# Optimization experiments

Hardware: AMD Instinct MI355X
Metric: run time of the kernel (lower is better)

## Reference

```python
import jax, jax.numpy as jnp
import numpy as np
import math

EMB, HEAD, B, S = 1024, 64, 4, 4096

def setup_inputs() -> dict:
    key = jax.random.key(0)
    ks = jax.random.split(key, 7)
    scale = 1.0 / math.sqrt(EMB)
    return {
        "x": jax.random.normal(ks[0], (B, S, EMB), dtype=jnp.float32),
        "Wq": jax.random.uniform(ks[1], (EMB, HEAD), jnp.float32, -scale, scale),
        "bq": jax.random.uniform(ks[2], (HEAD,), jnp.float32, -scale, scale),
        "Wk": jax.random.uniform(ks[3], (EMB, HEAD), jnp.float32, -scale, scale),
        "bk": jax.random.uniform(ks[4], (HEAD,), jnp.float32, -scale, scale),
        "Wv": jax.random.uniform(ks[5], (EMB, HEAD), jnp.float32, -scale, scale),
        "bv": jax.random.uniform(ks[6], (HEAD,), jnp.float32, -scale, scale),
    }

def reference(x, Wq, bq, Wk, bk, Wv, bv):
    # x: [B, S, E]
    q = x @ Wq + bq            # [B, S, H]
    k = x @ Wk + bk
    v = x @ Wv + bv
    scores = jnp.einsum('bqh,bkh->bqk', q, k) / math.sqrt(q.shape[-1])
    # causal mask: position q attends to k <= q
    s = x.shape[1]
    causal = jnp.tril(jnp.ones((s, s), dtype=bool))
    scores = jnp.where(causal, scores, -jnp.inf)
    attn = jax.nn.softmax(scores, axis=-1)
    return jnp.einsum('bqk,bkh->bqh', attn, v)
```

## Files before the change

kernel.cpp:

```cpp
#include <hip/hip_runtime.h>
#include <hip/hip_bf16.h>
#include <math.h>

#define EMB 1024
#define HEAD 64
#define NB 4
#define SEQ 4096
#define MTOT (NB * SEQ)
#define QSCALE (0.125f * 1.44269504088896f)

typedef __attribute__((ext_vector_type(8))) short bf16x8;
typedef __attribute__((ext_vector_type(4))) float f32x4;
typedef __attribute__((ext_vector_type(16))) float f32x16;

static __device__ __forceinline__ unsigned short f2b(float f) {
    union { float f; unsigned u; } v; v.f = f;
    unsigned r = v.u + 0x7FFFu + ((v.u >> 16) & 1u);
    return (unsigned short)(r >> 16);
}
static __device__ __forceinline__ float b2f(unsigned short u) {
    union { unsigned u; float f; } v; v.u = ((unsigned)u) << 16; return v.f;
}
static __device__ __forceinline__ unsigned pk2(float lo, float hi) {
    unsigned r;
    asm("v_cvt_pk_bf16_f32 %0, %1, %2" : "=v"(r) : "v"(lo), "v"(hi));
    return r;
}

__global__ void wt_kernel(const float* __restrict__ Wq, const float* __restrict__ Wk,
                          const float* __restrict__ Wv, unsigned short* __restrict__ Wt) {
    const int idx = blockIdx.x * 256 + threadIdx.x;
    const int m = idx >> 16;
    const int r = idx & 65535;
    const int n = r >> 10, k = r & 1023;
    const float* W = (m == 0) ? Wq : (m == 1) ? Wk : Wv;
    Wt[idx] = f2b(W[k * HEAD + n]);
}

__global__ __launch_bounds__(256) void proj_kernel(
    const float* __restrict__ x, const unsigned short* __restrict__ Wt3,
    const float* __restrict__ bq, const float* __restrict__ bk,
    const float* __restrict__ bv, unsigned short* __restrict__ qg,
    unsigned short* __restrict__ kb, unsigned short* __restrict__ vb) {
    __shared__ unsigned short Ax[32][72];
    __shared__ unsigned short Wl[192][72];

    const int tid = threadIdx.x;
    const int wave = tid >> 6, lane = tid & 63;
    const int li = lane & 15, lg = lane >> 4;
    const int rbase = blockIdx.x * 32;

    f32x4 acc[2][3];
#pragma unroll
    for (int m = 0; m < 2; ++m)
#pragma unroll
        for (int n = 0; n < 3; ++n) acc[m][n] = (f32x4){0.f, 0.f, 0.f, 0.f};

    const int xr = tid >> 3, xc = (tid & 7) * 8;

    for (int k0 = 0; k0 < EMB; k0 += 64) {
        __syncthreads();
        const float* xp = x + (size_t)(rbase + xr) * EMB + k0 + xc;
        const float4 t0 = *(const float4*)(xp);
        const float4 t1 = *(const float4*)(xp + 4);
        union { bf16x8 v; unsigned u[4]; } pa;
        pa.u[0] = pk2(t0.x, t0.y); pa.u[1] = pk2(t0.z, t0.w);
        pa.u[2] = pk2(t1.x, t1.y); pa.u[3] = pk2(t1.z, t1.w);
        *(bf16x8*)&Ax[xr][xc] = pa.v;
#pragma unroll
        for (int i = 0; i < 6; ++i) {
            const int chunk = tid + 256 * i;
            const int row = chunk >> 3, c8 = (chunk & 7) * 8;
            *(bf16x8*)&Wl[row][c8] = *(const bf16x8*)(Wt3 + (size_t)row * EMB + k0 + c8);
        }
        __syncthreads();

        const bf16x8 a0 = *(const bf16x8*)&Ax[li][lg * 8];
        const bf16x8 a1 = *(const bf16x8*)&Ax[li][32 + lg * 8];
        const bf16x8 a2 = *(const bf16x8*)&Ax[16 + li][lg * 8];
        const bf16x8 a3 = *(const bf16x8*)&Ax[16 + li][32 + lg * 8];
#pragma unroll
        for (int n = 0; n < 3; ++n) {
            const bf16x8 b0 = *(const bf16x8*)&Wl[(wave * 3 + n) * 16 + li][lg * 8];
            const bf16x8 b1 = *(const bf16x8*)&Wl[(wave * 3 + n) * 16 + li][32 + lg * 8];
            acc[0][n] = __builtin_amdgcn_mfma_f32_16x16x32_bf16(a0, b0, acc[0][n], 0, 0, 0);
            acc[0][n] = __builtin_amdgcn_mfma_f32_16x16x32_bf16(a1, b1, acc[0][n], 0, 0, 0);
            acc[1][n] = __builtin_amdgcn_mfma_f32_16x16x32_bf16(a2, b0, acc[1][n], 0, 0, 0);
            acc[1][n] = __builtin_amdgcn_mfma_f32_16x16x32_bf16(a3, b1, acc[1][n], 0, 0, 0);
        }
    }
#pragma unroll
    for (int m = 0; m < 2; ++m)
#pragma unroll
        for (int n = 0; n < 3; ++n) {
            const int f = wave * 3 + n;
            const int mat = f >> 2;
            const int nc = (f & 3) * 16 + li;
            const float bb = (mat == 0) ? bq[nc] : (mat == 1) ? bk[nc] : bv[nc];
#pragma unroll
            for (int r = 0; r < 4; ++r) {
                const int grow = rbase + m * 16 + lg * 4 + r;
                const float val = acc[m][n][r] + bb;
                const int bi = grow >> 12, si = grow & 4095;
                if (mat == 0) {
                    qg[(size_t)grow * HEAD + nc] = f2b(val * QSCALE);
                } else if (mat == 1) {
                    kb[((size_t)(bi * 2 + ((nc >> 3) & 1)) * 4 + (nc >> 4)) * (SEQ * 8)
                       + (size_t)si * 8 + (nc & 7)] = f2b(val);
                } else {
                    vb[((size_t)(bi * 512 + (si >> 3))) * 512 + (size_t)nc * 8 + (si & 7)] = f2b(val);
                }
            }
        }
}

template<int W64, int NWIN, int KMAX>
__global__ __launch_bounds__(256) void attn_kernel(
    const unsigned short* __restrict__ Qg, const unsigned short* __restrict__ Kb,
    const unsigned short* __restrict__ Vb, unsigned* __restrict__ pO,
    float* __restrict__ pML) {
    const int lane = threadIdx.x & 63;
    const int ql = lane & 31, h = lane >> 5;
    const int b = blockIdx.y;
    const int w = blockIdx.x * 4 + (threadIdx.x >> 6);
    int seg = 0;
#pragma unroll
    for (int kk = 1; kk < KMAX; ++kk)
        if (w >= 128 * kk - W64 * kk * (kk - 1)) seg = kk;
    const int Os = 128 * seg - W64 * seg * (seg - 1);
    const int qidx = 2 * W64 * seg + (w - Os);
    const int tdiag = qidx >> 1;
    const int qa0 = qidx * 32;
    const int t0 = W64 * seg;
    const int tend = (t0 + W64 < tdiag + 1) ? t0 + W64 : tdiag + 1;

    const size_t qb = (size_t)b * SEQ * HEAD;
    const unsigned short* kb0 = Kb + ((size_t)(b * 2 + h)) * 4 * (SEQ * 8);
    const unsigned short* vb0 = Vb + (size_t)b * 512 * 512;

    const unsigned short* qrow = Qg + qb + (size_t)(qa0 + ql) * HEAD + h * 8;
    bf16x8 qf[4];
#pragma unroll
    for (int s = 0; s < 4; ++s) qf[s] = *(const bf16x8*)(qrow + s * 16);

    f32x16 oa0, oa1;
#pragma unroll
    for (int r = 0; r < 16; ++r) { oa0[r] = 0.f; oa1[r] = 0.f; }
    float m = -1e30f, lsum = 0.f;

    bf16x8 kcur[2][4], knxt[2][4];
#pragma unroll
    for (int hh = 0; hh < 2; ++hh)
#pragma unroll
        for (int s = 0; s < 4; ++s)
            kcur[hh][s] = *(const bf16x8*)(kb0 + (size_t)s * (SEQ * 8)
                                           + ((size_t)t0 * 64 + 32 * hh + ql) * 8);

    for (int t = t0; t < tend; ++t) {
        bf16x8 vf[2][4];
#pragma unroll
        for (int dt = 0; dt < 2; ++dt)
#pragma unroll
            for (int cc = 0; cc < 4; ++cc)
                vf[dt][cc] = *(const bf16x8*)(vb0 + ((size_t)t * 8 + 2 * cc + h) * 512
                                              + (dt * 32 + ql) * 8);

        f32x16 st0, st1;
#pragma unroll
        for (int r = 0; r < 16; ++r) { st0[r] = 0.f; st1[r] = 0.f; }
        __builtin_amdgcn_s_setprio(1);
#pragma unroll
        for (int s = 0; s < 4; ++s) {
            st0 = __builtin_amdgcn_mfma_f32_32x32x16_bf16(kcur[0][s], qf[s], st0, 0, 0, 0);
            st1 = __builtin_amdgcn_mfma_f32_32x32x16_bf16(kcur[1][s], qf[s], st1, 0, 0, 0);
        }
        __builtin_amdgcn_s_setprio(0);

        if (t + 1 < tend) {
#pragma unroll
            for (int hh = 0; hh < 2; ++hh)
#pragma unroll
                for (int s = 0; s < 4; ++s)
                    knxt[hh][s] = *(const bf16x8*)(kb0 + (size_t)s * (SEQ * 8)
                                                   + ((size_t)(t + 1) * 64 + 32 * hh + ql) * 8);
        }

        if (t == tdiag) {
            if (qidx & 1) {
#pragma unroll
                for (int r = 0; r < 16; ++r) {
                    const int kvl = (r & 3) + 8 * (r >> 2) + 4 * h;
                    if (kvl > ql) st1[r] = -1e30f;
                }
            } else {
#pragma unroll
                for (int r = 0; r < 16; ++r) {
                    const int kvl = (r & 3) + 8 * (r >> 2) + 4 * h;
                    if (kvl > ql) st0[r] = -1e30f;
                    st1[r] = -1e30f;
                }
            }
        }
        float cm = -1e30f;
#pragma unroll
        for (int r = 0; r < 16; ++r) cm = fmaxf(cm, fmaxf(st0[r], st1[r]));
        cm = fmaxf(cm, __shfl_xor(cm, 32));
        if (!__all(cm - m <= 8.0f)) {
            const float mn = fmaxf(m, cm);
            const float sc = exp2f(m - mn);
            m = mn;
            lsum *= sc;
#pragma unroll
            for (int r = 0; r < 16; ++r) { oa0[r] *= sc; oa1[r] *= sc; }
        }
        float ls = 0.f;
#pragma unroll
        for (int r = 0; r < 16; ++r) {
            st0[r] = exp2f(st0[r] - m);
            st1[r] = exp2f(st1[r] - m);
            ls += st0[r] + st1[r];
        }
        lsum += ls;

        bf16x8 bfv[4];
#pragma unroll
        for (int hh = 0; hh < 2; ++hh) {
            unsigned w8[8];
#pragma unroll
            for (int tt = 0; tt < 8; ++tt)
                w8[tt] = hh ? pk2(st1[2 * tt], st1[2 * tt + 1])
                            : pk2(st0[2 * tt], st0[2 * tt + 1]);
            const unsigned xa0 = h ? w8[0] : w8[2];
            const unsigned va0 = __shfl_xor((int)xa0, 32);
            const unsigned xb0 = h ? w8[1] : w8[3];
            const unsigned vb_0 = __shfl_xor((int)xb0, 32);
            union { bf16x8 v; unsigned u[4]; } bbv;
            bbv.u[0] = h ? va0 : w8[0];
            bbv.u[1] = h ? vb_0 : w8[1];
            bbv.u[2] = h ? w8[2] : va0;
            bbv.u[3] = h ? w8[3] : vb_0;
            bfv[hh * 2] = bbv.v;
            const unsigned xa1 = h ? w8[4] : w8[6];
            const unsigned va1 = __shfl_xor((int)xa1, 32);
            const unsigned xb1 = h ? w8[5] : w8[7];
            const unsigned vb_1 = __shfl_xor((int)xb1, 32);
            bbv.u[0] = h ? va1 : w8[4];
            bbv.u[1] = h ? vb_1 : w8[5];
            bbv.u[2] = h ? w8[6] : va1;
            bbv.u[3] = h ? w8[7] : vb_1;
            bfv[hh * 2 + 1] = bbv.v;
        }
        __builtin_amdgcn_s_setprio(1);
#pragma unroll
        for (int cc = 0; cc < 4; ++cc) {
            oa0 = __builtin_amdgcn_mfma_f32_32x32x16_bf16(vf[0][cc], bfv[cc], oa0, 0, 0, 0);
            oa1 = __builtin_amdgcn_mfma_f32_32x32x16_bf16(vf[1][cc], bfv[cc], oa1, 0, 0, 0);
        }
        __builtin_amdgcn_s_setprio(0);

#pragma unroll
        for (int hh = 0; hh < 2; ++hh)
#pragma unroll
            for (int s = 0; s < 4; ++s)
                kcur[hh][s] = knxt[hh][s];
    }

    lsum += __shfl_xor(lsum, 32);
    const size_t gw = (size_t)b * NWIN + w;
    unsigned* po = pO + gw * 1024;
#pragma unroll
    for (int r = 0; r < 16; r += 2) {
        const int dp = ((r & 3) >> 1) + 4 * (r >> 2) + 2 * h;
        po[dp * 32 + ql] = pk2(oa0[r], oa0[r + 1]);
        po[(16 + dp) * 32 + ql] = pk2(oa1[r], oa1[r + 1]);
    }
    if (h == 0) {
        pML[gw * 64 + ql * 2] = m;
        pML[gw * 64 + ql * 2 + 1] = lsum;
    }
}

template<int W64, int NWIN>
__global__ __launch_bounds__(256) void merge_kernel(
    const unsigned* __restrict__ pO, const float* __restrict__ pML,
    float* __restrict__ out) {
    const int qidx = blockIdx.x, b = blockIdx.y;
    const int wcount = qidx / (2 * W64) + 1;
    const int t = threadIdx.x;
    const int ql = t & 31, g = t >> 5;

    float M = -1e30f;
    for (int k = 0; k < wcount; ++k) {
        const int Os = 128 * k - W64 * k * (k - 1);
        const size_t gw = (size_t)b * NWIN + Os + (qidx - 2 * W64 * k);
        M = fmaxf(M, pML[gw * 64 + ql * 2]);
    }
    float acc[8] = {0.f, 0.f, 0.f, 0.f, 0.f, 0.f, 0.f, 0.f};
    float L = 0.f;
    for (int k = 0; k < wcount; ++k) {
        const int Os = 128 * k - W64 * k * (k - 1);
        const size_t gw = (size_t)b * NWIN + Os + (qidx - 2 * W64 * k);
        const float mk = pML[gw * 64 + ql * 2];
        const float lk = pML[gw * 64 + ql * 2 + 1];
        const float wgt = exp2f(mk - M);
        L += wgt * lk;
#pragma unroll
        for (int i = 0; i < 4; ++i) {
            const unsigned u = pO[gw * 1024 + (size_t)(g * 4 + i) * 32 + ql];
            acc[2 * i] += wgt * b2f((unsigned short)(u & 0xFFFFu));
            acc[2 * i + 1] += wgt * b2f((unsigned short)(u >> 16));
        }
    }
    const float inv = 1.0f / L;
    float* op = out + ((size_t)b * SEQ + qidx * 32 + ql) * HEAD + g * 8;
    f32x4 o0 = {acc[0] * inv, acc[1] * inv, acc[2] * inv, acc[3] * inv};
    f32x4 o1 = {acc[4] * inv, acc[5] * inv, acc[6] * inv, acc[7] * inv};
    *(f32x4*)(op) = o0;
    *(f32x4*)(op + 4) = o1;
}

extern "C" void kernel_launch(void* const* d_in, const int* in_sizes, int n_in,
                              void* d_out, int out_size, void* d_ws, size_t ws_size,
                              hipStream_t stream) {
    const float* x  = (const float*)d_in[0];
    const float* Wq = (const float*)d_in[1];
    const float* bq = (const float*)d_in[2];
    const float* Wk = (const float*)d_in[3];
    const float* bk = (const float*)d_in[4];
    const float* Wv = (const float*)d_in[5];
    const float* bv = (const float*)d_in[6];

    unsigned short* Wt = (unsigned short*)d_ws;
    unsigned short* qg = Wt + 3 * HEAD * EMB;
    unsigned short* kb = qg + (size_t)MTOT * HEAD;
    unsigned short* vb = kb + (size_t)MTOT * HEAD;
    unsigned* pO = (unsigned*)(vb + (size_t)MTOT * HEAD);
    const size_t base_shorts = (size_t)3 * HEAD * EMB + (size_t)3 * MTOT * HEAD;

    wt_kernel<<<dim3(768), dim3(256), 0, stream>>>(Wq, Wk, Wv, Wt);
    proj_kernel<<<dim3(MTOT / 32), dim3(256), 0, stream>>>(x, Wt, bq, bk, bv, qg, kb, vb);

    const size_t need4 = base_shorts * 2 + (size_t)NB * 1088 * (1024 * 4 + 64 * 4);
    if (ws_size >= need4) {
        float* pML = (float*)(pO + (size_t)NB * 1088 * 1024);
        attn_kernel<4, 1088, 16><<<dim3(272, NB), dim3(256), 0, stream>>>(qg, kb, vb, pO, pML);
        merge_kernel<4, 1088><<<dim3(128, NB), dim3(256), 0, stream>>>(pO, pML, (float*)d_out);
    } else {
        float* pML = (float*)(pO + (size_t)NB * 576 * 1024);
        attn_kernel<8, 576, 8><<<dim3(144, NB), dim3(256), 0, stream>>>(qg, kb, vb, pO, pML);
        merge_kernel<8, 576><<<dim3(128, NB), dim3(256), 0, stream>>>(pO, pML, (float*)d_out);
    }
}
```

Measured before the change: 72.09 us.

## Stage projection outputs through LDS and split attention into finer KV windows

After: 102.2 us. 1.42x slower.

```diff
diff --git a/kernel.cpp b/kernel.cpp
--- a/kernel.cpp
+++ b/kernel.cpp
@@ -89,6 +89,9 @@
             acc[1][n] = __builtin_amdgcn_mfma_f32_16x16x32_bf16(a3, b1, acc[1][n], 0, 0, 0);
         }
     }
+
+    __syncthreads();
+    unsigned short (*R)[208] = (unsigned short (*)[208])&Wl[0][0];
 #pragma unroll
     for (int m = 0; m < 2; ++m)
 #pragma unroll
@@ -99,30 +102,44 @@
             const float bb = (mat == 0) ? bq[nc] : (mat == 1) ? bk[nc] : bv[nc];
 #pragma unroll
             for (int r = 0; r < 4; ++r) {
-                const int grow = rbase + m * 16 + lg * 4 + r;
                 const float val = acc[m][n][r] + bb;
-                const int bi = grow >> 12, si = grow & 4095;
-                if (mat == 0) {
-                    qg[(size_t)grow * HEAD + nc] = f2b(val * QSCALE);
-                } else if (mat == 1) {
-                    kb[((size_t)(bi * 2 + ((nc >> 3) & 1)) * 4 + (nc >> 4)) * (SEQ * 8)
-                       + (size_t)si * 8 + (nc & 7)] = f2b(val);
-                } else {
-                    vb[((size_t)(bi * 512 + (si >> 3))) * 512 + (size_t)nc * 8 + (si & 7)] = f2b(val);
-                }
+                R[m * 16 + lg * 4 + r][f * 16 + li] = f2b(mat == 0 ? val * QSCALE : val);
             }
         }
+    __syncthreads();
+
+    const int bi = rbase >> 12, si0 = rbase & 4095;
+    {
+        const int row = tid >> 3, c8 = (tid & 7) * 8;
+        *(bf16x8*)(qg + (size_t)(rbase + row) * HEAD + c8) = *(const bf16x8*)&R[row][c8];
+    }
+    {
+        const int plane = tid >> 5, row = tid & 31;
+        const int s = plane >> 1, hb = plane & 1;
+        *(bf16x8*)(kb + ((size_t)((bi * 2 + hb) * 4 + s)) * (SEQ * 8)
+                   + (size_t)(si0 + row) * 8)
+            = *(const bf16x8*)&R[row][64 + s * 16 + hb * 8];
+    }
+    {
+        const int kvc = tid >> 6, nc = tid & 63;
+        bf16x8 v;
+#pragma unroll
+        for (int jj = 0; jj < 8; ++jj) v[jj] = (short)R[kvc * 8 + jj][128 + nc];
+        *(bf16x8*)(vb + ((size_t)(bi * 512 + (si0 >> 3) + kvc)) * 512 + nc * 8) = v;
+    }
 }
 
 template<int W64, int NWIN, int KMAX>
-__global__ __launch_bounds__(256) void attn_kernel(
+__global__ __launch_bounds__(128) void attn_kernel(
     const unsigned short* __restrict__ Qg, const unsigned short* __restrict__ Kb,
     const unsigned short* __restrict__ Vb, unsigned* __restrict__ pO,
     float* __restrict__ pML) {
     const int lane = threadIdx.x & 63;
     const int ql = lane & 31, h = lane >> 5;
-    const int b = blockIdx.y;
-    const int w = blockIdx.x * 4 + (threadIdx.x >> 6);
+    const int g = blockIdx.x;
+    const int b = (g & 7) >> 1;
+    const int bx = (g >> 3) * 2 + (g & 1);
+    const int w = bx * 2 + (threadIdx.x >> 6);
     int seg = 0;
 #pragma unroll
     for (int kk = 1; kk < KMAX; ++kk)
@@ -340,14 +357,14 @@
     wt_kernel<<<dim3(768), dim3(256), 0, stream>>>(Wq, Wk, Wv, Wt);
     proj_kernel<<<dim3(MTOT / 32), dim3(256), 0, stream>>>(x, Wt, bq, bk, bv, qg, kb, vb);
 
-    const size_t need4 = base_shorts * 2 + (size_t)NB * 1088 * (1024 * 4 + 64 * 4);
-    if (ws_size >= need4) {
+    const size_t need2 = base_shorts * 2 + (size_t)NB * 2112 * (1024 * 4 + 64 * 4);
+    if (ws_size >= need2) {
+        float* pML = (float*)(pO + (size_t)NB * 2112 * 1024);
+        attn_kernel<2, 2112, 32><<<dim3(2112 / 2 * NB), dim3(128), 0, stream>>>(qg, kb, vb, pO, pML);
+        merge_kernel<2, 2112><<<dim3(128, NB), dim3(256), 0, stream>>>(pO, pML, (float*)d_out);
+    } else {
         float* pML = (float*)(pO + (size_t)NB * 1088 * 1024);
-        attn_kernel<4, 1088, 16><<<dim3(272, NB), dim3(256), 0, stream>>>(qg, kb, vb, pO, pML);
+        attn_kernel<4, 1088, 16><<<dim3(1088 / 2 * NB), dim3(128), 0, stream>>>(qg, kb, vb, pO, pML);
         merge_kernel<4, 1088><<<dim3(128, NB), dim3(256), 0, stream>>>(pO, pML, (float*)d_out);
-    } else {
-        float* pML = (float*)(pO + (size_t)NB * 576 * 1024);
-        attn_kernel<8, 576, 8><<<dim3(144, NB), dim3(256), 0, stream>>>(qg, kb, vb, pO, pML);
-        merge_kernel<8, 576><<<dim3(128, NB), dim3(256), 0, stream>>>(pO, pML, (float*)d_out);
-    }
-}
+    }
+}
```
